# Performance work log

Measured on AMD Instinct MI355X. Metric: run time of the kernel, lower is better.

## Reference

```python
import jax, jax.numpy as jnp
import numpy as np

D_MODEL = 1024
RANK = 256
INIT_ALPHA = 0.5


def setup_inputs() -> dict:
    key = jax.random.key(0)
    ks = jax.random.split(key, 12)
    D, R = D_MODEL, RANK
    s = 0.02
    return {
        "x": jax.random.normal(ks[0], (4, 2048, D), dtype=jnp.float32),
        "Wq": jax.random.normal(ks[1], (D, D), dtype=jnp.float32) * s,
        "Wk": jax.random.normal(ks[2], (D, D), dtype=jnp.float32) * s,
        "Wo": jax.random.normal(ks[3], (D, D), dtype=jnp.float32) * s,
        "U_b": jax.random.normal(ks[4], (D, R), dtype=jnp.float32) * s,
        "V_b": jax.random.normal(ks[5], (D, R), dtype=jnp.float32) * s,
        "W_b": jax.random.normal(ks[6], (D, R), dtype=jnp.float32) * s,
        "bias_b": jnp.zeros((D,), dtype=jnp.float32),
        "U_t": jax.random.normal(ks[7], (D, R), dtype=jnp.float32) * s,
        "V_t": jax.random.normal(ks[8], (D, R), dtype=jnp.float32) * s,
        "W_t": jax.random.normal(ks[9], (D, R), dtype=jnp.float32) * s,
        "X_t": jax.random.normal(ks[10], (D, R), dtype=jnp.float32) * s,
        "bias_t": jnp.zeros((D,), dtype=jnp.float32),
        "alpha": jnp.asarray(INIT_ALPHA, dtype=jnp.float32),
    }


def reference(x, Wq, Wk, Wo, U_b, V_b, W_b, bias_b, U_t, V_t, W_t, X_t, bias_t, alpha):
    # Math identical to the original O(T^2 D) materialization (attention_mask=None path),
    # reduced to causal cumulative sums: sum_{j<=i} (q_i * k_j) = q_i * cumsum_j(k_j).
    B, T, D = x.shape
    Q = x @ Wq.T                      # [B,T,D] (nn.Linear: x @ W^T)
    K = x @ Wk.T
    counts = jnp.arange(1, T + 1, dtype=x.dtype)[None, :, None]  # [1,T,1]
    Z = jnp.cumsum(x, axis=1) / counts  # causal cumulative mean [B,T,D]

    # Bilinear: sum_{j<=i} ((Q_i V_b) * (K_j W_b)) U_b^T + bias_b (per j)
    a_b = Q @ V_b                     # [B,T,R]
    c_b = jnp.cumsum(K @ W_b, axis=1) # [B,T,R] causal sum over j
    bil = (a_b * c_b) @ U_b.T         # [B,T,D]

    # Trilinear: sum_{j<=i} ((Q_i V_t) * (K_j W_t) * (Z_i X_t)) U_t^T + bias_t
    a_t = Q @ V_t
    c_t = jnp.cumsum(K @ W_t, axis=1)
    z_t = Z @ X_t
    tri = (a_t * z_t * c_t) @ U_t.T   # [B,T,D]

    # Per-i division by n_valid = i+1; the per-(i,j) biases average back to themselves.
    out = (bil + alpha * tri) / counts + (bias_b + alpha * bias_t)
    return out @ Wo.T                 # W_O (dropout=0 -> identity)
```

## Files before the change

### kernel.cpp

```cpp
#include <hip/hip_runtime.h>

#define NBATCH  4
#define TSEQ    2048
#define MROWS   8192
#define NCAT    1280
#define NE      512

#define OFF_WQT   0u
#define OFF_WKT   524288u
#define OFF_WOB   1048576u
#define OFF_VCT   1572864u
#define OFF_WCT   1835008u
#define OFF_UCT   2097152u
#define OFF_B2    2359296u
#define OFF_PB    2360320u
#define OFF_GB    3015680u
#define OFF_Y     3277824u
#define OFF_SCR   13763584u
#define OFF_XB    13861888u
#define OFF_EB    OFF_XB

typedef __attribute__((ext_vector_type(8))) short bf16x8;
typedef __attribute__((ext_vector_type(4))) float f32x4;

__device__ __forceinline__ unsigned short f2bf(float f) {
  union { float f; unsigned u; } v; v.f = f;
  return (unsigned short)((v.u + 0x7fff + ((v.u >> 16) & 1)) >> 16);
}
__device__ __forceinline__ float bf2f(unsigned short u) {
  union { unsigned u; float f; } v; v.u = ((unsigned)u) << 16;
  return v.f;
}

__device__ __forceinline__ void gload16(const void* g, void* l) {
  __builtin_amdgcn_global_load_lds(
      (const __attribute__((address_space(1))) unsigned*)g,
      (__attribute__((address_space(3))) unsigned*)l, 16, 0, 0);
}

template <int EPI, int OBF, int CS>
__device__ __forceinline__ void mfma_tile(
    const short* __restrict__ A, const short* __restrict__ B, void* __restrict__ Cv,
    int K, int ldA, int ldB, int ldC, int m0, int n0,
    const float* __restrict__ bias, float* __restrict__ scr, short* L) {
  const int tid = threadIdx.x;
  const int l = tid & 63;
  const int wv = tid >> 6;
  const int wm = (wv >> 1) * 64, wn = (wv & 1) * 64;
  const int sr = tid >> 2;
  const int sc4 = tid & 3;
  const int arow = wm + (l & 15), brow = wn + (l & 15);
  const int kq = l >> 4;

  f32x4 acc[4][4] = {};

#define STAGE(k0, buf) do {                                                  \
    short* As_ = L + (buf) * 8192;                                           \
    short* Bs_ = As_ + 4096;                                                 \
    _Pragma("unroll")                                                        \
    for (int p = 0; p < 2; ++p) {                                            \
      const int r = p * 64 + sr;                                             \
      const int sw = (sc4 ^ (r & 3)) * 8;                                    \
      gload16(A + (size_t)(m0 + r) * ldA + (k0) + sw, As_ + r * 32 + sc4 * 8); \
      gload16(B + (size_t)(n0 + r) * ldB + (k0) + sw, Bs_ + r * 32 + sc4 * 8); \
    }                                                                        \
  } while (0)

#define COMPUTE(buf) do {                                                    \
    short* As_ = L + (buf) * 8192;                                           \
    short* Bs_ = As_ + 4096;                                                 \
    bf16x8 af[4], bfr[4];                                                    \
    _Pragma("unroll")                                                        \
    for (int m = 0; m < 4; ++m) {                                            \
      const int r = arow + m * 16;                                           \
      af[m] = *(const bf16x8*)&As_[r * 32 + ((kq ^ (r & 3)) * 8)];           \
    }                                                                        \
    _Pragma("unroll")                                                        \
    for (int n = 0; n < 4; ++n) {                                            \
      const int r = brow + n * 16;                                           \
      bfr[n] = *(const bf16x8*)&Bs_[r * 32 + ((kq ^ (r & 3)) * 8)];          \
    }                                                                        \
    _Pragma("unroll")                                                        \
    for (int m = 0; m < 4; ++m)                                              \
      _Pragma("unroll")                                                      \
      for (int n = 0; n < 4; ++n)                                            \
        acc[m][n] = __builtin_amdgcn_mfma_f32_16x16x32_bf16(af[m], bfr[n], acc[m][n], 0, 0, 0); \
  } while (0)

  STAGE(0, 0);
  STAGE(32, 1);
  const int nt = K >> 5;
  int cur = 0, nxt = 2;
  for (int t = 0; t < nt; ++t) {
    if (t + 2 < nt) {
      STAGE((t + 2) << 5, nxt);
      asm volatile("s_waitcnt vmcnt(8)" ::: "memory");
    } else if (t + 1 < nt) {
      asm volatile("s_waitcnt vmcnt(4)" ::: "memory");
    } else {
      asm volatile("s_waitcnt vmcnt(0)" ::: "memory");
    }
    asm volatile("s_barrier" ::: "memory");
    COMPUTE(cur);
    asm volatile("s_barrier" ::: "memory");
    cur = (cur == 2) ? 0 : cur + 1;
    nxt = (nxt == 2) ? 0 : nxt + 1;
  }
#undef STAGE
#undef COMPUTE

  const int cc = wn + (l & 15);
  const int crb = wm + (l >> 4) * 4;
#pragma unroll
  for (int m = 0; m < 4; ++m) {
#pragma unroll
    for (int j = 0; j < 4; ++j) {
      const int gm = m0 + crb + m * 16 + j;
      float inv = 1.0f;
      if (EPI) inv = 1.0f / (float)((gm & (TSEQ - 1)) + 1);
#pragma unroll
      for (int n = 0; n < 4; ++n) {
        const int gn = n0 + cc + n * 16;
        float v = acc[m][n][j];
        if (EPI) v = v * inv + bias[gn];
        if (OBF) ((short*)Cv)[(size_t)gm * ldC + gn] = (short)f2bf(v);
        else     ((float*)Cv)[(size_t)gm * ldC + gn] = v;
      }
    }
  }
  if (CS && n0 >= 512) {
    const int bb = (m0 + wm) >> 11;
    const int seg = ((m0 + wm) & (TSEQ - 1)) >> 6;
    float* sp = scr + (size_t)(bb * 32 + seg) * 768 + (n0 - 512);
#pragma unroll
    for (int n = 0; n < 4; ++n) {
      float s = 0.f;
#pragma unroll
      for (int m = 0; m < 4; ++m)
#pragma unroll
        for (int j = 0; j < 4; ++j) s += acc[m][n][j];
      s += __shfl_xor(s, 16, 64);
      s += __shfl_xor(s, 32, 64);
      if (l < 16) sp[cc + n * 16] = s;
    }
  }
}

__device__ __forceinline__ void xcd_swizzle(int& bx, int& by) {
  const int gx = gridDim.x;
  const int nwg = gx * gridDim.y;
  const int n = by * gx + bx;
  const int q = nwg >> 3;
  const int s = (n & 7) * q + (n >> 3);
  bx = s % gx; by = s / gx;
}

template <int EPI, int OBF, int CS>
__global__ __launch_bounds__(256) void mfma_nt(
    const short* __restrict__ A, const short* __restrict__ B,
    void* __restrict__ C, int K, int ldA, int ldB, int ldC,
    const float* __restrict__ bias, float* __restrict__ scr) {
  __shared__ short L[24576];
  int bx = blockIdx.x, by = blockIdx.y;
  xcd_swizzle(bx, by);
  mfma_tile<EPI, OBF, CS>(A, B, C, K, ldA, ldB, ldC,
                          by * 128, bx * 128, bias, scr, L);
}

__global__ __launch_bounds__(256) void prep_mfma(
    const short* __restrict__ VCT, const short* __restrict__ WQT,
    const short* __restrict__ WCT, const short* __restrict__ WKT,
    const short* __restrict__ WOB, const short* __restrict__ UCT,
    short* __restrict__ Pb, short* __restrict__ Gb) {
  __shared__ short L[24576];
  const int g = blockIdx.x >> 5, t = blockIdx.x & 31;
  if (g == 0)
    mfma_tile<0, 1, 0>(VCT, WQT, Pb, 1024, 1024, 1024, 1024,
                       (t >> 3) * 128, (t & 7) * 128, nullptr, nullptr, L);
  else if (g == 1)
    mfma_tile<0, 1, 0>(WCT, WKT, Pb + (size_t)512 * 1024, 1024, 1024, 1024, 1024,
                       (t >> 3) * 128, (t & 7) * 128, nullptr, nullptr, L);
  else
    mfma_tile<0, 1, 0>(WOB, UCT, Gb, 1024, 1024, 1024, 512,
                       (t >> 2) * 128, (t & 3) * 128, nullptr, nullptr, L);
}

__global__ __launch_bounds__(256) void prep_all(
    const float* __restrict__ Vb, const float* __restrict__ Vt,
    const float* __restrict__ Wb, const float* __restrict__ Wt,
    const float* __restrict__ Ub, const float* __restrict__ Ut,
    const float* __restrict__ Xt, const float* __restrict__ Wq,
    const float* __restrict__ Wk, const float* __restrict__ Wo,
    const float* __restrict__ x,
    const float* __restrict__ bias_b, const float* __restrict__ bias_t,
    const float* __restrict__ alpha_p,
    short* __restrict__ VCT, short* __restrict__ WCT, short* __restrict__ UCT,
    short* __restrict__ PbXt, short* __restrict__ WQT, short* __restrict__ WKT,
    short* __restrict__ WOB, short* __restrict__ xb, float* __restrict__ b2) {
  const int bid = blockIdx.x;
  const int tid = threadIdx.x;
  if (bid >= 10176) {
    const float al = *alpha_p;
    const int d = bid - 10176;
    float s = 0.f;
    for (int e = tid; e < 1024; e += 256)
      s += Wo[(size_t)d * 1024 + e] * (bias_b[e] + al * bias_t[e]);
    __shared__ float red[256];
    red[tid] = s; __syncthreads();
    for (int off = 128; off > 0; off >>= 1) {
      if (tid < off) red[tid] += red[tid + off];
      __syncthreads();
    }
    if (tid == 0) b2[d] = red[0];
    return;
  }
  if (bid >= 960) {
    const size_t j = ((size_t)(bid - 960) * 256 + tid) * 4;
    const int isWo = j < 1048576u;
    const float* s = isWo ? &Wo[j] : &x[j - 1048576u];
    const float4 v = *(const float4*)s;
    ushort4 o;
    o.x = f2bf(v.x); o.y = f2bf(v.y); o.z = f2bf(v.z); o.w = f2bf(v.w);
    unsigned short* dst = (unsigned short*)(isWo ? WOB : xb);
    *(ushort4*)&dst[isWo ? j : j - 1048576u] = o;
    return;
  }
  const float* src; short* O; int r0, d0, c0, ldS;
  if (bid < 384) {
    const int z = bid >> 7, t = bid & 127;
    r0 = (t >> 4) * 64; d0 = (t & 15) * 64; ldS = 256;
    const float* S0 = z == 0 ? Vb : z == 1 ? Wb : Ub;
    const float* S1 = z == 0 ? Vt : z == 1 ? Wt : Ut;
    O = z == 0 ? VCT : z == 1 ? WCT : UCT;
    src = (r0 < 256) ? S0 : S1; c0 = r0 & 255;
  } else if (bid < 448) {
    const int t = bid - 384;
    r0 = (t >> 4) * 64; d0 = (t & 15) * 64; ldS = 256;
    src = Xt; c0 = r0; O = PbXt;
  } else {
    const int t = bid - 448;
    const int w = t >> 8, tt = t & 255;
    r0 = (tt >> 4) * 64; d0 = (tt & 15) * 64; ldS = 1024;
    src = w ? Wk : Wq; O = w ? WKT : WQT; c0 = r0;
  }
  __shared__ float Ts[64][65];
  const int lr = tid >> 4;
  const int lc = (tid & 15) * 4;
#pragma unroll
  for (int p = 0; p < 4; ++p) {
    const int row = lr + p * 16;
    const float4 v = *(const float4*)&src[(size_t)(d0 + row) * ldS + c0 + lc];
    Ts[row][lc + 0] = v.x; Ts[row][lc + 1] = v.y;
    Ts[row][lc + 2] = v.z; Ts[row][lc + 3] = v.w;
  }
  __syncthreads();
#pragma unroll
  for (int p = 0; p < 4; ++p) {
    const int ri = lr + p * 16;
    ushort4 o;
    o.x = f2bf(Ts[lc + 0][ri]); o.y = f2bf(Ts[lc + 1][ri]);
    o.z = f2bf(Ts[lc + 2][ri]); o.w = f2bf(Ts[lc + 3][ri]);
    *(ushort4*)&((unsigned short*)O)[(size_t)(r0 + ri) * 1024 + d0 + lc] = o;
  }
}

__global__ void cumsum_s2(float* __restrict__ scr) {
  const int lane = threadIdx.x;
  const int cg = blockIdx.x, b = blockIdx.z;
  const int c = cg * 64 + lane;
  float run = 0.f;
  for (int seg = 0; seg < 32; ++seg) {
    const size_t idx = (size_t)(b * 32 + seg) * 768 + c;
    const float v = scr[idx];
    scr[idx] = run;
    run += v;
  }
}

#define LOADR(s, t) {                                                   \
    const unsigned short* p_ = yb + (size_t)(t) * NCAT;                 \
    ab##s = bf2f(p_[c2]);        at##s = bf2f(p_[256 + c2]);            \
    cb##s = bf2f(p_[512 + c2]);  ct##s = bf2f(p_[768 + c2]);            \
    zt##s = bf2f(p_[1024 + c2]); }
#define STEPR(s, t) {                                                   \
    run_cb += cb##s; run_ct += ct##s; run_zt += zt##s;                  \
    const float inv_ = 1.0f / (float)(segbase + (t) + 1);               \
    unsigned short* er_ = Eb + (row0 + (t)) * 512;                      \
    er_[c2]       = f2bf(ab##s * run_cb);                               \
    er_[256 + c2] = f2bf(al * at##s * (run_zt * inv_) * run_ct); }
__global__ __launch_bounds__(256) void scan_combine(
    const unsigned short* __restrict__ Y, const float* __restrict__ scr,
    unsigned short* __restrict__ Eb, const float* __restrict__ alpha_p) {
  const float al = *alpha_p;
  const int c2 = threadIdx.x;
  const int seg = blockIdx.x, b = blockIdx.y;
  const int segbase = seg * 64;
  const float* sc = scr + (size_t)(b * 32 + seg) * 768;
  float run_cb = sc[c2];
  float run_ct = sc[256 + c2];
  float run_zt = sc[512 + c2];
  const size_t row0 = (size_t)(b * TSEQ + segbase);
  const unsigned short* yb = Y + row0 * NCAT;
  float ab0, at0, cb0, ct0, zt0, ab1, at1, cb1, ct1, zt1;
  float ab2, at2, cb2, ct2, zt2, ab3, at3, cb3, ct3, zt3;
  float ab4, at4, cb4, ct4, zt4, ab5, at5, cb5, ct5, zt5;
  float ab6, at6, cb6, ct6, zt6, ab7, at7, cb7, ct7, zt7;
  LOADR(0, 0) LOADR(1, 1) LOADR(2, 2) LOADR(3, 3)
  LOADR(4, 4) LOADR(5, 5) LOADR(6, 6) LOADR(7, 7)
  for (int t = 0; t < 64; t += 8) {
    STEPR(0, t + 0) if (t + 8 < 64)  LOADR(0, t + 8)
    STEPR(1, t + 1) if (t + 9 < 64)  LOADR(1, t + 9)
    STEPR(2, t + 2) if (t + 10 < 64) LOADR(2, t + 10)
    STEPR(3, t + 3) if (t + 11 < 64) LOADR(3, t + 11)
    STEPR(4, t + 4) if (t + 12 < 64) LOADR(4, t + 12)
    STEPR(5, t + 5) if (t + 13 < 64) LOADR(5, t + 13)
    STEPR(6, t + 6) if (t + 14 < 64) LOADR(6, t + 14)
    STEPR(7, t + 7) if (t + 15 < 64) LOADR(7, t + 15)
  }
}
#undef LOADR
#undef STEPR

extern "C" void kernel_launch(void* const* d_in, const int* in_sizes, int n_in,
                              void* d_out, int out_size, void* d_ws, size_t ws_size,
                              hipStream_t stream) {
  const float* x      = (const float*)d_in[0];
  const float* Wq     = (const float*)d_in[1];
  const float* Wk     = (const float*)d_in[2];
  const float* Wo     = (const float*)d_in[3];
  const float* Ub     = (const float*)d_in[4];
  const float* Vb     = (const float*)d_in[5];
  const float* Wb     = (const float*)d_in[6];
  const float* bias_b = (const float*)d_in[7];
  const float* Ut     = (const float*)d_in[8];
  const float* Vt     = (const float*)d_in[9];
  const float* Wt     = (const float*)d_in[10];
  const float* Xt     = (const float*)d_in[11];
  const float* bias_t = (const float*)d_in[12];
  const float* alpha  = (const float*)d_in[13];
  float* out = (float*)d_out;
  float* ws  = (float*)d_ws;

  short* WQT = (short*)(ws + OFF_WQT);
  short* WKT = (short*)(ws + OFF_WKT);
  short* WOB = (short*)(ws + OFF_WOB);
  short* VCT = (short*)(ws + OFF_VCT);
  short* WCT = (short*)(ws + OFF_WCT);
  short* UCT = (short*)(ws + OFF_UCT);
  float* b2  = ws + OFF_B2;
  short* Pb  = (short*)(ws + OFF_PB);
  short* Gb  = (short*)(ws + OFF_GB);
  unsigned short* Yb = (unsigned short*)(ws + OFF_Y);
  float* scr = ws + OFF_SCR;
  short* xb  = (short*)(ws + OFF_XB);
  short* Eb  = (short*)(ws + OFF_EB);

  prep_all<<<11200, 256, 0, stream>>>(Vb, Vt, Wb, Wt, Ub, Ut, Xt, Wq, Wk, Wo, x,
                                      bias_b, bias_t, alpha,
                                      VCT, WCT, UCT, Pb + (size_t)1024 * 1024,
                                      WQT, WKT, WOB, xb, b2);
  prep_mfma<<<96, 256, 0, stream>>>(VCT, WQT, WCT, WKT, WOB, UCT, Pb, Gb);
  mfma_nt<0, 1, 1><<<dim3(NCAT / 128, MROWS / 128), 256, 0, stream>>>(
      xb, Pb, Yb, 1024, 1024, 1024, NCAT, nullptr, scr);
  cumsum_s2<<<dim3(12, 1, NBATCH), 64, 0, stream>>>(scr);
  scan_combine<<<dim3(32, NBATCH), 256, 0, stream>>>(Yb, scr, (unsigned short*)Eb, alpha);
  mfma_nt<1, 0, 0><<<dim3(1024 / 128, MROWS / 128), 256, 0, stream>>>(
      Eb, Gb, out, 512, 512, 512, 1024, b2, nullptr);
}
```

Before: 204.1 us.

## Widen GEMM K-tile to 64, move x conversion into prep2, fold segment prefix into scan

The MFMA GEMM tile now stages 64-wide K slices with double buffering, replacing 32-wide slices with triple buffering, and uses an 8-chunk XOR swizzle and 64KB LDS. This halves the number of barrier iterations. Conversion of x to bf16 moves out of prep_all and runs in the same launch as the weight-product GEMMs, so it overlaps with those few blocks. The separate cumsum_s2 kernel is removed, and each scan_combine block sums the preceding segment totals itself. This cuts one launch but adds redundant reads, and the larger LDS footprint may lower occupancy.

Result: faster. 196.7 us (-3.6%).

```diff
diff --git a/kernel.cpp b/kernel.cpp
--- a/kernel.cpp
+++ b/kernel.cpp
@@ -47,64 +47,61 @@
   const int l = tid & 63;
   const int wv = tid >> 6;
   const int wm = (wv >> 1) * 64, wn = (wv & 1) * 64;
-  const int sr = tid >> 2;
-  const int sc4 = tid & 3;
+  const int srow = tid >> 3;
+  const int schk = tid & 7;
   const int arow = wm + (l & 15), brow = wn + (l & 15);
   const int kq = l >> 4;
 
   f32x4 acc[4][4] = {};
 
 #define STAGE(k0, buf) do {                                                  \
-    short* As_ = L + (buf) * 8192;                                           \
-    short* Bs_ = As_ + 4096;                                                 \
+    short* As_ = L + (buf) * 16384;                                          \
+    short* Bs_ = As_ + 8192;                                                 \
     _Pragma("unroll")                                                        \
-    for (int p = 0; p < 2; ++p) {                                            \
-      const int r = p * 64 + sr;                                             \
-      const int sw = (sc4 ^ (r & 3)) * 8;                                    \
-      gload16(A + (size_t)(m0 + r) * ldA + (k0) + sw, As_ + r * 32 + sc4 * 8); \
-      gload16(B + (size_t)(n0 + r) * ldB + (k0) + sw, Bs_ + r * 32 + sc4 * 8); \
+    for (int p = 0; p < 4; ++p) {                                            \
+      const int r = p * 32 + srow;                                           \
+      const int sw = (schk ^ (r & 7)) * 8;                                   \
+      gload16(A + (size_t)(m0 + r) * ldA + (k0) + sw, As_ + r * 64 + schk * 8); \
+      gload16(B + (size_t)(n0 + r) * ldB + (k0) + sw, Bs_ + r * 64 + schk * 8); \
     }                                                                        \
   } while (0)
 
 #define COMPUTE(buf) do {                                                    \
-    short* As_ = L + (buf) * 8192;                                           \
-    short* Bs_ = As_ + 4096;                                                 \
-    bf16x8 af[4], bfr[4];                                                    \
+    short* As_ = L + (buf) * 16384;                                          \
+    short* Bs_ = As_ + 8192;                                                 \
     _Pragma("unroll")                                                        \
-    for (int m = 0; m < 4; ++m) {                                            \
-      const int r = arow + m * 16;                                           \
-      af[m] = *(const bf16x8*)&As_[r * 32 + ((kq ^ (r & 3)) * 8)];           \
+    for (int h = 0; h < 2; ++h) {                                            \
+      bf16x8 af[4], bfr[4];                                                  \
+      _Pragma("unroll")                                                      \
+      for (int m = 0; m < 4; ++m) {                                          \
+        const int r = arow + m * 16;                                         \
+        af[m] = *(const bf16x8*)&As_[r * 64 + (((h * 4 + kq) ^ (r & 7)) * 8)]; \
+      }                                                                      \
+      _Pragma("unroll")                                                      \
+      for (int n = 0; n < 4; ++n) {                                          \
+        const int r = brow + n * 16;                                         \
+        bfr[n] = *(const bf16x8*)&Bs_[r * 64 + (((h * 4 + kq) ^ (r & 7)) * 8)]; \
+      }                                                                      \
+      _Pragma("unroll")                                                      \
+      for (int m = 0; m < 4; ++m)                                            \
+        _Pragma("unroll")                                                    \
+        for (int n = 0; n < 4; ++n)                                          \
+          acc[m][n] = __builtin_amdgcn_mfma_f32_16x16x32_bf16(af[m], bfr[n], acc[m][n], 0, 0, 0); \
     }                                                                        \
-    _Pragma("unroll")                                                        \
-    for (int n = 0; n < 4; ++n) {                                            \
-      const int r = brow + n * 16;                                           \
-      bfr[n] = *(const bf16x8*)&Bs_[r * 32 + ((kq ^ (r & 3)) * 8)];          \
-    }                                                                        \
-    _Pragma("unroll")                                                        \
-    for (int m = 0; m < 4; ++m)                                              \
-      _Pragma("unroll")                                                      \
-      for (int n = 0; n < 4; ++n)                                            \
-        acc[m][n] = __builtin_amdgcn_mfma_f32_16x16x32_bf16(af[m], bfr[n], acc[m][n], 0, 0, 0); \
   } while (0)
 
   STAGE(0, 0);
-  STAGE(32, 1);
-  const int nt = K >> 5;
-  int cur = 0, nxt = 2;
+  const int nt = K >> 6;
   for (int t = 0; t < nt; ++t) {
-    if (t + 2 < nt) {
-      STAGE((t + 2) << 5, nxt);
+    if (t + 1 < nt) {
+      STAGE((t + 1) << 6, (t + 1) & 1);
       asm volatile("s_waitcnt vmcnt(8)" ::: "memory");
-    } else if (t + 1 < nt) {
-      asm volatile("s_waitcnt vmcnt(4)" ::: "memory");
     } else {
       asm volatile("s_waitcnt vmcnt(0)" ::: "memory");
     }
     asm volatile("s_barrier" ::: "memory");
-    COMPUTE(cur);
+    COMPUTE(t & 1);
     asm volatile("s_barrier" ::: "memory");
-    cur = (cur == 2) ? 0 : cur + 1;
-    nxt = (nxt == 2) ? 0 : nxt + 1;
   }
 #undef STAGE
 #undef COMPUTE
@@ -160,20 +157,30 @@
     const short* __restrict__ A, const short* __restrict__ B,
     void* __restrict__ C, int K, int ldA, int ldB, int ldC,
     const float* __restrict__ bias, float* __restrict__ scr) {
-  __shared__ short L[24576];
+  __shared__ short L[32768];
   int bx = blockIdx.x, by = blockIdx.y;
   xcd_swizzle(bx, by);
   mfma_tile<EPI, OBF, CS>(A, B, C, K, ldA, ldB, ldC,
                           by * 128, bx * 128, bias, scr, L);
 }
 
-__global__ __launch_bounds__(256) void prep_mfma(
+__global__ __launch_bounds__(256) void prep2(
     const short* __restrict__ VCT, const short* __restrict__ WQT,
     const short* __restrict__ WCT, const short* __restrict__ WKT,
     const short* __restrict__ WOB, const short* __restrict__ UCT,
-    short* __restrict__ Pb, short* __restrict__ Gb) {
-  __shared__ short L[24576];
-  const int g = blockIdx.x >> 5, t = blockIdx.x & 31;
+    short* __restrict__ Pb, short* __restrict__ Gb,
+    const float* __restrict__ x, short* __restrict__ xb) {
+  __shared__ short L[32768];
+  const int bid = blockIdx.x;
+  if (bid >= 96) {
+    const size_t j = ((size_t)(bid - 96) * 256 + threadIdx.x) * 4;
+    const float4 v = *(const float4*)&x[j];
+    ushort4 o;
+    o.x = f2bf(v.x); o.y = f2bf(v.y); o.z = f2bf(v.z); o.w = f2bf(v.w);
+    *(ushort4*)&((unsigned short*)xb)[j] = o;
+    return;
+  }
+  const int g = bid >> 5, t = bid & 31;
   if (g == 0)
     mfma_tile<0, 1, 0>(VCT, WQT, Pb, 1024, 1024, 1024, 1024,
                        (t >> 3) * 128, (t & 7) * 128, nullptr, nullptr, L);
@@ -191,17 +198,16 @@
     const float* __restrict__ Ub, const float* __restrict__ Ut,
     const float* __restrict__ Xt, const float* __restrict__ Wq,
     const float* __restrict__ Wk, const float* __restrict__ Wo,
-    const float* __restrict__ x,
     const float* __restrict__ bias_b, const float* __restrict__ bias_t,
     const float* __restrict__ alpha_p,
     short* __restrict__ VCT, short* __restrict__ WCT, short* __restrict__ UCT,
     short* __restrict__ PbXt, short* __restrict__ WQT, short* __restrict__ WKT,
-    short* __restrict__ WOB, short* __restrict__ xb, float* __restrict__ b2) {
+    short* __restrict__ WOB, float* __restrict__ b2) {
   const int bid = blockIdx.x;
   const int tid = threadIdx.x;
-  if (bid >= 10176) {
+  if (bid >= 1984) {
     const float al = *alpha_p;
-    const int d = bid - 10176;
+    const int d = bid - 1984;
     float s = 0.f;
     for (int e = tid; e < 1024; e += 256)
       s += Wo[(size_t)d * 1024 + e] * (bias_b[e] + al * bias_t[e]);
@@ -216,13 +222,10 @@
   }
   if (bid >= 960) {
     const size_t j = ((size_t)(bid - 960) * 256 + tid) * 4;
-    const int isWo = j < 1048576u;
-    const float* s = isWo ? &Wo[j] : &x[j - 1048576u];
-    const float4 v = *(const float4*)s;
+    const float4 v = *(const float4*)&Wo[j];
     ushort4 o;
     o.x = f2bf(v.x); o.y = f2bf(v.y); o.z = f2bf(v.z); o.w = f2bf(v.w);
-    unsigned short* dst = (unsigned short*)(isWo ? WOB : xb);
-    *(ushort4*)&dst[isWo ? j : j - 1048576u] = o;
+    *(ushort4*)&((unsigned short*)WOB)[j] = o;
     return;
   }
   const float* src; short* O; int r0, d0, c0, ldS;
@@ -261,19 +264,6 @@
     o.x = f2bf(Ts[lc + 0][ri]); o.y = f2bf(Ts[lc + 1][ri]);
     o.z = f2bf(Ts[lc + 2][ri]); o.w = f2bf(Ts[lc + 3][ri]);
     *(ushort4*)&((unsigned short*)O)[(size_t)(r0 + ri) * 1024 + d0 + lc] = o;
-  }
-}
-
-__global__ void cumsum_s2(float* __restrict__ scr) {
-  const int lane = threadIdx.x;
-  const int cg = blockIdx.x, b = blockIdx.z;
-  const int c = cg * 64 + lane;
-  float run = 0.f;
-  for (int seg = 0; seg < 32; ++seg) {
-    const size_t idx = (size_t)(b * 32 + seg) * 768 + c;
-    const float v = scr[idx];
-    scr[idx] = run;
-    run += v;
   }
 }
 
@@ -295,10 +285,11 @@
   const int c2 = threadIdx.x;
   const int seg = blockIdx.x, b = blockIdx.y;
   const int segbase = seg * 64;
-  const float* sc = scr + (size_t)(b * 32 + seg) * 768;
-  float run_cb = sc[c2];
-  float run_ct = sc[256 + c2];
-  float run_zt = sc[512 + c2];
+  float run_cb = 0.f, run_ct = 0.f, run_zt = 0.f;
+  for (int s = 0; s < seg; ++s) {
+    const float* sr = scr + (size_t)(b * 32 + s) * 768;
+    run_cb += sr[c2]; run_ct += sr[256 + c2]; run_zt += sr[512 + c2];
+  }
   const size_t row0 = (size_t)(b * TSEQ + segbase);
   const unsigned short* yb = Y + row0 * NCAT;
   float ab0, at0, cb0, ct0, zt0, ab1, at1, cb1, ct1, zt1;
@@ -355,14 +346,13 @@
   short* xb  = (short*)(ws + OFF_XB);
   short* Eb  = (short*)(ws + OFF_EB);
 
-  prep_all<<<11200, 256, 0, stream>>>(Vb, Vt, Wb, Wt, Ub, Ut, Xt, Wq, Wk, Wo, x,
-                                      bias_b, bias_t, alpha,
-                                      VCT, WCT, UCT, Pb + (size_t)1024 * 1024,
-                                      WQT, WKT, WOB, xb, b2);
-  prep_mfma<<<96, 256, 0, stream>>>(VCT, WQT, WCT, WKT, WOB, UCT, Pb, Gb);
+  prep_all<<<3008, 256, 0, stream>>>(Vb, Vt, Wb, Wt, Ub, Ut, Xt, Wq, Wk, Wo,
+                                     bias_b, bias_t, alpha,
+                                     VCT, WCT, UCT, Pb + (size_t)1024 * 1024,
+                                     WQT, WKT, WOB, b2);
+  prep2<<<8288, 256, 0, stream>>>(VCT, WQT, WCT, WKT, WOB, UCT, Pb, Gb, x, xb);
   mfma_nt<0, 1, 1><<<dim3(NCAT / 128, MROWS / 128), 256, 0, stream>>>(
       xb, Pb, Yb, 1024, 1024, 1024, NCAT, nullptr, scr);
-  cumsum_s2<<<dim3(12, 1, NBATCH), 64, 0, stream>>>(scr);
   scan_combine<<<dim3(32, NBATCH), 256, 0, stream>>>(Yb, scr, (unsigned short*)Eb, alpha);
   mfma_nt<1, 0, 0><<<dim3(1024 / 128, MROWS / 128), 256, 0, stream>>>(
       Eb, Gb, out, 512, 512, 512, 1024, b2, nullptr);
```
